# Kernel optimization log

Measured on AMD Instinct MI355X. Metric: run time of the kernel, lower is better.

Reference implementation:

```python
import jax, jax.numpy as jnp
import numpy as np

# model dims (DeepSeekV2-Lite-like, reduced expert count)
H = 2048      # hidden_dim
NH = 16       # num_heads
NOPE = 128    # qk_nope_head_dim
ROPE = 64     # qk_rope_head_dim (interleaved rotary)
VD = 128      # v_head_dim
QL = 1536     # q_lora_rank
KVL = 512     # kv_lora_rank
E = 8         # num routed experts
TOPK = 2      # num_experts_per_token
MI = 512      # moe_intermediate_dim
SH_I = 2 * MI # num_shared_experts * moe_intermediate_dim
B = 1
S = 2048
T = B * S
EPS = 1e-6
MOE_SCALE = 1.0  # gating_scaling_factor


def setup_inputs() -> dict:
    key = jax.random.key(0)
    ks = jax.random.split(key, 16)
    def w(k, shape):
        return jax.random.normal(k, shape, dtype=jnp.float32) * 0.02
    # interleaved rotary tables: one angle per (even,odd) pair
    half = ROPE // 2
    pos = jnp.arange(S, dtype=jnp.float32)
    inv_freq = 1.0 / (10000.0 ** (jnp.arange(half, dtype=jnp.float32) * 2.0 / ROPE))
    ang = pos[:, None] * inv_freq[None, :]              # [S, half]
    sin = jnp.tile(jnp.sin(ang), (B, 1))                # [T, half]
    cos = jnp.tile(jnp.cos(ang), (B, 1))
    return {
        "x": jax.random.normal(ks[0], (T, H), jnp.float32),
        "skip": jax.random.normal(ks[1], (T, H), jnp.float32),
        "rotary_sin": sin,
        "rotary_cos": cos,
        "ln1_w": jnp.ones((H,), jnp.float32),
        "ln2_w": jnp.ones((H,), jnp.float32),
        "w_qa": w(ks[2], (QL, H)),
        "qa_norm_w": jnp.ones((QL,), jnp.float32),
        "w_qb": w(ks[3], (NH * (NOPE + ROPE), QL)),
        "w_kva": w(ks[4], (KVL + ROPE, H)),
        "kva_norm_w": jnp.ones((KVL,), jnp.float32),
        "w_kb": w(ks[5], (NH * NOPE, KVL)),
        "w_vb": w(ks[6], (NH * VD, KVL)),
        "w_o": w(ks[7], (H, NH * VD)),
        "gate_w": w(ks[8], (E, H)),
        "moe_up_w": w(ks[9], (E, 2 * MI, H)),
        "moe_down_w": w(ks[10], (E, H, MI)),
        "shared_up_w": w(ks[11], (2 * SH_I, H)),
        "shared_down_w": w(ks[12], (H, SH_I)),
        "batch": B,
    }


def _rms(v, w):
    return v * jax.lax.rsqrt(jnp.mean(v * v, axis=-1, keepdims=True) + EPS) * w


def _rope_interleaved(v, sin, cos):
    # v: [T, nh, ROPE]; sin/cos: [T, ROPE//2]; rotate (even, odd) pairs
    x1, x2 = v[..., 0::2], v[..., 1::2]
    s, c = sin[:, None, :], cos[:, None, :]
    o1 = x1 * c - x2 * s
    o2 = x1 * s + x2 * c
    return jnp.stack([o1, o2], axis=-1).reshape(v.shape)


def reference(x, skip, rotary_sin, rotary_cos, ln1_w, ln2_w, w_qa, qa_norm_w,
              w_qb, w_kva, kva_norm_w, w_kb, w_vb, w_o, gate_w,
              moe_up_w, moe_down_w, shared_up_w, shared_down_w, batch):
    Tt = x.shape[0]
    Sq = Tt // batch
    # SkipRMSNorm #1
    x1 = x + skip
    n1 = _rms(x1, ln1_w)
    # ---- MLA attention (prefill path, decoding_batches=0) ----
    qa = _rms(n1 @ w_qa.T, qa_norm_w)                               # [T, QL]
    q = (qa @ w_qb.T).reshape(Tt, NH, NOPE + ROPE)
    q_nope, q_pe = q[..., :NOPE], q[..., NOPE:]
    q_pe = _rope_interleaved(q_pe, rotary_sin, rotary_cos)
    kv = n1 @ w_kva.T                                               # [T, KVL+ROPE]
    ckv = _rms(kv[:, :KVL], kva_norm_w)
    k_pe = _rope_interleaved(kv[:, KVL:][:, None, :], rotary_sin, rotary_cos)  # [T,1,ROPE]
    k_nope = (ckv @ w_kb.T).reshape(Tt, NH, NOPE)
    v = (ckv @ w_vb.T).reshape(Tt, NH, VD)
    qf = jnp.concatenate([q_nope, q_pe], -1).reshape(batch, Sq, NH, NOPE + ROPE)
    kf = jnp.concatenate([k_nope, jnp.broadcast_to(k_pe, (Tt, NH, ROPE))], -1)
    kf = kf.reshape(batch, Sq, NH, NOPE + ROPE)
    vf = v.reshape(batch, Sq, NH, VD)
    scale = 1.0 / np.sqrt(NOPE + ROPE)
    scores = jnp.einsum('bqhd,bkhd->bhqk', qf, kf) * scale
    causal = jnp.tril(jnp.ones((Sq, Sq), bool))
    scores = jnp.where(causal[None, None], scores, jnp.float32(-1e30))
    p = jax.nn.softmax(scores, axis=-1)
    o = jnp.einsum('bhqk,bkhd->bqhd', p, vf).reshape(Tt, NH * VD)
    attn = o @ w_o.T
    # SkipRMSNorm #2
    x2 = x1 + attn
    n2 = _rms(x2, ln2_w)
    # ---- MoE FFN: softmax gate, greedy top-k, normalized probs ----
    probs = jax.nn.softmax(n2 @ gate_w.T, axis=-1)                  # [T, E]
    tv, ti = jax.lax.top_k(probs, TOPK)
    tv = tv / jnp.sum(tv, axis=-1, keepdims=True) * MOE_SCALE
    routed = jnp.zeros_like(n2)
    for e in range(E):  # fixed small expert count; masked dense dispatch
        we = jnp.sum(tv * (ti == e), axis=-1)                       # [T]
        h = n2 @ moe_up_w[e].T                                      # [T, 2*MI]
        h = jax.nn.silu(h[:, :MI]) * h[:, MI:]
        routed = routed + we[:, None] * (h @ moe_down_w[e].T)
    # shared experts (dense swiglu MLP)
    hs = n2 @ shared_up_w.T
    hs = jax.nn.silu(hs[:, :SH_I]) * hs[:, SH_I:]
    ffn = routed + hs @ shared_down_w.T
    return (x2, ffn)
```

## Files before the change

### kernel.cpp

```cpp
#include <hip/hip_runtime.h>
#include <hip/hip_bf16.h>

#define H 2048
#define NH 16
#define NOPE 128
#define ROPE_D 64
#define DQK 192
#define VD 128
#define QL 1536
#define KVL 512
#define NE 8
#define MI_D 512
#define SHI 1024
#define EPS 1e-6f
#define MAXA 5120

typedef unsigned short bfu;
typedef short bf16x8 __attribute__((ext_vector_type(8)));
typedef float f32x4 __attribute__((ext_vector_type(4)));

#define MFMA16(a, b, c) __builtin_amdgcn_mfma_f32_16x16x32_bf16(a, b, c, 0, 0, 0)

#define BAR_PLAIN()   asm volatile("s_barrier" ::: "memory")
#define BAR_LGKM0()   asm volatile("s_waitcnt lgkmcnt(0)\n\ts_barrier" ::: "memory")
#define BAR_VM4()     asm volatile("s_waitcnt vmcnt(4)\n\ts_barrier" ::: "memory")
#define BAR_VM0()     asm volatile("s_waitcnt vmcnt(0)\n\ts_barrier" ::: "memory")

__device__ __forceinline__ float bf2f(bfu u) {
    union { unsigned int i; float f; } w; w.i = ((unsigned int)u) << 16; return w.f;
}
__device__ __forceinline__ bfu f2bf(float f) {
    union { float f; unsigned int i; } u; u.f = f;
    return (bfu)((u.i + 0x7fffu + ((u.i >> 16) & 1u)) >> 16);
}

__device__ __forceinline__ void async16(const bfu* g, bfu* l) {
    __builtin_amdgcn_global_load_lds((const __attribute__((address_space(1))) void*)g,
                                     (__attribute__((address_space(3))) void*)l, 16, 0, 0);
}

__device__ __forceinline__ float blk_sum(float v) {
    __shared__ float sb[4];
    for (int o = 32; o > 0; o >>= 1) v += __shfl_down(v, o, 64);
    int lane = threadIdx.x & 63, w = threadIdx.x >> 6;
    __syncthreads();
    if (lane == 0) sb[w] = v;
    __syncthreads();
    return sb[0] + sb[1] + sb[2] + sb[3];
}

struct GemmSeg {
    const bfu* A; const bfu* B; void* C; void* C2;
    const int* aidx; const int* eid;
    long bstride;
    int N, K, ldm3, mode, nx, ntiles;
};

__device__ __forceinline__ void gemm_body(const bfu* __restrict__ A, const bfu* __restrict__ B,
                                          void* __restrict__ Cv, void* __restrict__ Cv2,
                                          int N, int K, int ldm3, int mode,
                                          const int* __restrict__ aidx,
                                          const int* __restrict__ eid, long bstride,
                                          int bx, int by,
                                          bfu* sAb, bfu* sBb) {
    bfu (*sA)[128 * 32] = (bfu (*)[128 * 32])sAb;
    bfu (*sB)[128 * 32] = (bfu (*)[128 * 32])sBb;
    const int tid = threadIdx.x;
    const int lane = tid & 63, w = tid >> 6;
    const int quad = lane >> 4, li = lane & 15;
    const int m0 = by * 128, n0 = bx * 128;
    const bfu* Bp = B + (eid ? (size_t)eid[by] * bstride : 0);

    const int l4 = lane >> 2;
    const int lg = lane & 3;
    const int kc = lg ^ ((lane >> 3) & 3);
    int r0 = m0 + w * 32 + l4, r1 = r0 + 16;
    if (aidx) { r0 = aidx[r0]; r1 = aidx[r1]; }
    const bfu* gA0 = A + (size_t)r0 * K + kc * 8;
    const bfu* gA1 = A + (size_t)r1 * K + kc * 8;
    const bfu* gB0 = Bp + (size_t)(n0 + w * 32 + l4) * K + kc * 8;
    const bfu* gB1 = gB0 + (size_t)16 * K;
    const int oA0 = (w * 32) * 32, oA1 = (w * 32 + 16) * 32;

    const int wm = (w >> 1) * 64, wn = (w & 1) * 64;
    const int fg = (quad ^ ((li >> 1) & 3)) * 8;
    int oa[4], ob[4];
#pragma unroll
    for (int t4 = 0; t4 < 4; ++t4) {
        oa[t4] = (wm + t4 * 16 + li) * 32 + fg;
        ob[t4] = (wn + t4 * 16 + li) * 32 + fg;
    }
    f32x4 acc[4][4];
#pragma unroll
    for (int i = 0; i < 4; ++i)
#pragma unroll
        for (int j = 0; j < 4; ++j) acc[i][j] = (f32x4){0.f, 0.f, 0.f, 0.f};

    const int nb = K / 32;
    async16(gA0, &sA[0][oA0]); async16(gA1, &sA[0][oA1]);
    async16(gB0, &sB[0][oA0]); async16(gB1, &sB[0][oA1]);
    async16(gA0 + 32, &sA[1][oA0]); async16(gA1 + 32, &sA[1][oA1]);
    async16(gB0 + 32, &sB[1][oA0]); async16(gB1 + 32, &sB[1][oA1]);

    int cur = 0;
    for (int it = 0; it < nb; ++it) {
        if (it < nb - 1) { BAR_VM4(); } else { BAR_VM0(); }
        bf16x8 av[4], bv[4];
#pragma unroll
        for (int t4 = 0; t4 < 4; ++t4) av[t4] = *(const bf16x8*)&sA[cur][oa[t4]];
#pragma unroll
        for (int t4 = 0; t4 < 4; ++t4) bv[t4] = *(const bf16x8*)&sB[cur][ob[t4]];
        if (it + 2 < nb) {
            const int k1 = (it + 2) * 32;
            int nxt = cur + 2; if (nxt >= 3) nxt -= 3;
            async16(gA0 + k1, &sA[nxt][oA0]); async16(gA1 + k1, &sA[nxt][oA1]);
            async16(gB0 + k1, &sB[nxt][oA0]); async16(gB1 + k1, &sB[nxt][oA1]);
        }
#pragma unroll
        for (int mt = 0; mt < 4; ++mt)
#pragma unroll
            for (int nt = 0; nt < 4; ++nt)
                acc[mt][nt] = MFMA16(av[mt], bv[nt], acc[mt][nt]);
        if (++cur >= 3) cur = 0;
    }

#pragma unroll
    for (int mt = 0; mt < 4; ++mt)
#pragma unroll
        for (int nt = 0; nt < 4; ++nt) {
            int row = m0 + wm + mt * 16 + quad * 4;
            int col = n0 + wn + nt * 16 + li;
            if (mode == 0) {
                float* C = (float*)Cv;
#pragma unroll
                for (int r = 0; r < 4; ++r) C[(size_t)(row + r) * N + col] = acc[mt][nt][r];
            } else if (mode == 1) {
                bfu* C = (bfu*)Cv;
#pragma unroll
                for (int r = 0; r < 4; ++r) C[(size_t)(row + r) * N + col] = f2bf(acc[mt][nt][r]);
            } else {
                if (n0 < 2048) {
                    bfu* C = (bfu*)Cv;
#pragma unroll
                    for (int r = 0; r < 4; ++r) C[(size_t)(row + r) * 2048 + col] = f2bf(acc[mt][nt][r]);
                } else {
                    bfu* C2 = (bfu*)Cv2;
                    ushort4 u;
                    u.x = f2bf(acc[mt][nt][0]); u.y = f2bf(acc[mt][nt][1]);
                    u.z = f2bf(acc[mt][nt][2]); u.w = f2bf(acc[mt][nt][3]);
                    *(ushort4*)(C2 + (size_t)(col - 2048) * ldm3 + row) = u;
                }
            }
        }
}

__global__ __launch_bounds__(256) void gemm_multi(GemmSeg s0, GemmSeg s1) {
    __shared__ bfu sA[3][128 * 32];
    __shared__ bfu sB[3][128 * 32];
    int b = blockIdx.x;
    if (b < s0.ntiles) {
        gemm_body(s0.A, s0.B, s0.C, s0.C2, s0.N, s0.K, s0.ldm3, s0.mode,
                  s0.aidx, s0.eid, s0.bstride, b % s0.nx, b / s0.nx, &sA[0][0], &sB[0][0]);
    } else {
        int lb = b - s0.ntiles;
        gemm_body(s1.A, s1.B, s1.C, s1.C2, s1.N, s1.K, s1.ldm3, s1.mode,
                  s1.aidx, s1.eid, s1.bstride, lb % s1.nx, lb / s1.nx, &sA[0][0], &sB[0][0]);
    }
}

struct CastArgs {
    const float* s[10];
    bfu* d[10];
    unsigned start[11];
    int pad[10];
};
__global__ __launch_bounds__(256) void k_cast_all(CastArgs a) {
    unsigned g = blockIdx.x * 256 + threadIdx.x;
    if (g >= a.start[10]) return;
    int id = 0;
#pragma unroll
    for (int i = 1; i < 10; ++i) if (g >= a.start[i]) id = i;
    size_t i16 = (size_t)(g - a.start[id]) * 16;
    ushort4 u[4] = {};
    if (!a.pad[id] || (i16 >> 11) < 576) {
        const float* s = a.s[id];
#pragma unroll
        for (int j = 0; j < 4; ++j) {
            float4 x = *(const float4*)(s + i16 + j * 4);
            u[j].x = f2bf(x.x); u[j].y = f2bf(x.y); u[j].z = f2bf(x.z); u[j].w = f2bf(x.w);
        }
    }
    bfu* d = a.d[id];
#pragma unroll
    for (int j = 0; j < 4; ++j) *(ushort4*)(d + i16 + j * 4) = u[j];
}

__global__ __launch_bounds__(256) void k_add_rms(const float* __restrict__ x, const float* __restrict__ skip,
                                                 const float* __restrict__ w,
                                                 float* __restrict__ x1, bfu* __restrict__ n1b) {
    int t = blockIdx.x;
    size_t base = (size_t)t * H;
    float loc[8]; float ss = 0.f;
#pragma unroll
    for (int i = 0; i < 8; ++i) {
        int c = threadIdx.x + i * 256;
        float v = x[base + c] + skip[base + c];
        loc[i] = v; ss += v * v;
        x1[base + c] = v;
    }
    float tot = blk_sum(ss);
    float r = rsqrtf(tot / (float)H + EPS);
#pragma unroll
    for (int i = 0; i < 8; ++i) {
        int c = threadIdx.x + i * 256;
        n1b[base + c] = f2bf(loc[i] * r * w[c]);
    }
}

__global__ __launch_bounds__(256) void k_qkv_post(const bfu* __restrict__ qkv,
                                                  const float* __restrict__ qa_nw,
                                                  const float* __restrict__ kva_nw,
                                                  const float* __restrict__ sin_, const float* __restrict__ cos_,
                                                  bfu* __restrict__ qab, bfu* __restrict__ ckv,
                                                  bfu* __restrict__ kpe) {
    int t = blockIdx.x;
    const bfu* row = qkv + (size_t)t * 2176;
    float qa[6]; float ss1 = 0.f;
#pragma unroll
    for (int i = 0; i < 6; ++i) {
        float v = bf2f(row[threadIdx.x + i * 256]); qa[i] = v; ss1 += v * v;
    }
    float v0 = bf2f(row[1536 + threadIdx.x]), v1 = bf2f(row[1792 + threadIdx.x]);
    float s1 = blk_sum(ss1);
    float s2 = blk_sum(v0 * v0 + v1 * v1);
    float r1 = rsqrtf(s1 / (float)QL + EPS);
    float r2 = rsqrtf(s2 / 512.f + EPS);
#pragma unroll
    for (int i = 0; i < 6; ++i) {
        int c = threadIdx.x + i * 256;
        qab[(size_t)t * QL + c] = f2bf(qa[i] * r1 * qa_nw[c]);
    }
    ckv[(size_t)t * 512 + threadIdx.x]       = f2bf(v0 * r2 * kva_nw[threadIdx.x]);
    ckv[(size_t)t * 512 + threadIdx.x + 256] = f2bf(v1 * r2 * kva_nw[threadIdx.x + 256]);
    if (threadIdx.x < 32) {
        int p = threadIdx.x;
        float x1v = bf2f(row[2048 + 2 * p]), x2v = bf2f(row[2048 + 2 * p + 1]);
        float s = sin_[t * 32 + p], c = cos_[t * 32 + p];
        kpe[(size_t)t * 64 + 2 * p]     = f2bf(x1v * c - x2v * s);
        kpe[(size_t)t * 64 + 2 * p + 1] = f2bf(x1v * s + x2v * c);
    }
}

__global__ __launch_bounds__(256) void k_flash_mfma(const bfu* __restrict__ qb,
                                                    const bfu* __restrict__ kn,
                                                    const bfu* __restrict__ kpe,
                                                    const bfu* __restrict__ vt,
                                                    bfu* __restrict__ O,
                                                    const float* __restrict__ rsin,
                                                    const float* __restrict__ rcos, int T) {
    __shared__ bfu Ks[64 * 200];
    __shared__ bfu VtL[2][128 * 32];
    __shared__ bfu P[64 * 72];
    const int tid = threadIdx.x;
    const int lane = tid & 63, w = tid >> 6;
    const int quad = lane >> 4, li = lane & 15;
    const int q0 = ((int)gridDim.x - 1 - (int)blockIdx.x) * 64;
    const int h = blockIdx.y;
    const float scale = 0.07216878364870322f;

    bf16x8 qf[6];
    {
        int qrow = q0 + w * 16 + li;
        const bfu* qp = qb + ((size_t)qrow * NH + h) * DQK;
#pragma unroll
        for (int s6 = 0; s6 < 6; ++s6) {
            bf16x8 v = *(const bf16x8*)(qp + s6 * 32 + quad * 8);
            if (s6 >= 4) {
                int pb = (s6 - 4) * 16 + quad * 4;
#pragma unroll
                for (int j = 0; j < 4; ++j) {
                    float x1 = bf2f((bfu)v[2 * j]), x2 = bf2f((bfu)v[2 * j + 1]);
                    float s = rsin[qrow * 32 + pb + j], c = rcos[qrow * 32 + pb + j];
                    v[2 * j]     = (short)f2bf(x1 * c - x2 * s);
                    v[2 * j + 1] = (short)f2bf(x1 * s + x2 * c);
                }
            }
            qf[s6] = v;
        }
    }
    f32x4 accO[8];
#pragma unroll
    for (int i = 0; i < 8; ++i) accO[i] = (f32x4){0.f, 0.f, 0.f, 0.f};
    float lrow[4] = {0.f, 0.f, 0.f, 0.f};

    int kr[6], kg[6];
#pragma unroll
    for (int it = 0; it < 6; ++it) { int G = tid + it * 256; kr[it] = G / 24; kg[it] = G % 24; }
    int vn[4], vgl[4], vkc[4];
#pragma unroll
    for (int it = 0; it < 4; ++it) {
        int idx = tid + it * 256; vn[it] = idx >> 3; vgl[it] = idx & 7;
        vkc[it] = (vgl[it] & 4) | ((vgl[it] & 3) ^ ((vn[it] >> 1) & 3));
    }
    bf16x8 kreg[6], vreg[4];
#pragma unroll
    for (int it = 0; it < 6; ++it)
        kreg[it] = (kg[it] < 16) ? *(const bf16x8*)(kn + (size_t)kr[it] * (NH * 128) + h * 128 + kg[it] * 8)
                                 : *(const bf16x8*)(kpe + (size_t)kr[it] * 64 + (kg[it] - 16) * 8);
#pragma unroll
    for (int it = 0; it < 4; ++it)
        vreg[it] = *(const bf16x8*)(vt + (size_t)(h * 128 + vn[it]) * T + vkc[it] * 8);

    const int fgv = (quad ^ ((li >> 1) & 3)) * 8;
    const int kend = q0 + 64;
    for (int k0 = 0; k0 < kend; k0 += 64) {
        BAR_PLAIN();
#pragma unroll
        for (int it = 0; it < 6; ++it) *(bf16x8*)(Ks + kr[it] * 200 + kg[it] * 8) = kreg[it];
#pragma unroll
        for (int it = 0; it < 4; ++it)
            *(bf16x8*)(VtL[vgl[it] >> 2] + vn[it] * 32 + (vgl[it] & 3) * 8) = vreg[it];
        if (k0 + 64 < kend) {
            int k1 = k0 + 64;
#pragma unroll
            for (int it = 0; it < 6; ++it)
                kreg[it] = (kg[it] < 16) ? *(const bf16x8*)(kn + (size_t)(k1 + kr[it]) * (NH * 128) + h * 128 + kg[it] * 8)
                                         : *(const bf16x8*)(kpe + (size_t)(k1 + kr[it]) * 64 + (kg[it] - 16) * 8);
#pragma unroll
            for (int it = 0; it < 4; ++it)
                vreg[it] = *(const bf16x8*)(vt + (size_t)(h * 128 + vn[it]) * T + k1 + vkc[it] * 8);
        }
        BAR_LGKM0();
        f32x4 s[4];
#pragma unroll
        for (int ct = 0; ct < 4; ++ct) {
            f32x4 a = (f32x4){0.f, 0.f, 0.f, 0.f};
#pragma unroll
            for (int s6 = 0; s6 < 6; ++s6) {
                bf16x8 kf = *(const bf16x8*)(Ks + (ct * 16 + li) * 200 + s6 * 32 + quad * 8);
                a = MFMA16(qf[s6], kf, a);
            }
            s[ct] = a;
        }
#pragma unroll
        for (int ct = 0; ct < 4; ++ct)
#pragma unroll
            for (int r = 0; r < 4; ++r) {
                int row = q0 + w * 16 + quad * 4 + r;
                float p = (k0 + ct * 16 + li <= row) ? __expf(s[ct][r] * scale) : 0.f;
                s[ct][r] = p;
                lrow[r] += p;
            }
#pragma unroll
        for (int ct = 0; ct < 4; ++ct)
#pragma unroll
            for (int r = 0; r < 4; ++r)
                P[(w * 16 + quad * 4 + r) * 72 + ct * 16 + li] = f2bf(s[ct][r]);
        bf16x8 pf[2];
#pragma unroll
        for (int ks = 0; ks < 2; ++ks)
            pf[ks] = *(const bf16x8*)(P + (w * 16 + li) * 72 + ks * 32 + quad * 8);
#pragma unroll
        for (int v8 = 0; v8 < 8; ++v8)
#pragma unroll
            for (int ks = 0; ks < 2; ++ks) {
                bf16x8 vf = *(const bf16x8*)(VtL[ks] + (v8 * 16 + li) * 32 + fgv);
                accO[v8] = MFMA16(pf[ks], vf, accO[v8]);
            }
    }
#pragma unroll
    for (int r = 0; r < 4; ++r) {
        float l = lrow[r];
        l += __shfl_xor(l, 1); l += __shfl_xor(l, 2);
        l += __shfl_xor(l, 4); l += __shfl_xor(l, 8);
        lrow[r] = 1.0f / l;
    }
#pragma unroll
    for (int v8 = 0; v8 < 8; ++v8)
#pragma unroll
        for (int r = 0; r < 4; ++r) {
            float val = accO[v8][r] * lrow[r];
            O[(size_t)(q0 + w * 16 + quad * 4 + r) * (NH * 128) + h * 128 + v8 * 16 + li] = f2bf(val);
        }
}

__global__ __launch_bounds__(256) void k_x2_n2(const float* __restrict__ x1, const bfu* __restrict__ attn,
                                               const float* __restrict__ ln2w, float* __restrict__ outx2,
                                               bfu* __restrict__ n2b, const float* __restrict__ gw,
                                               int* __restrict__ eidx, float* __restrict__ wts,
                                               int* __restrict__ cnt) {
    int t = blockIdx.x;
    size_t base = (size_t)t * H;
    float loc[8]; float ss = 0.f;
#pragma unroll
    for (int i = 0; i < 8; ++i) {
        int c = threadIdx.x + i * 256;
        float vv = x1[base + c] + bf2f(attn[base + c]);
        loc[i] = vv; ss += vv * vv;
        outx2[base + c] = vv;
    }
    float tot = blk_sum(ss);
    float r = rsqrtf(tot / (float)H + EPS);
    float pe[NE] = {0.f, 0.f, 0.f, 0.f, 0.f, 0.f, 0.f, 0.f};
#pragma unroll
    for (int i = 0; i < 8; ++i) {
        int c = threadIdx.x + i * 256;
        float nv = loc[i] * r * ln2w[c];
        n2b[base + c] = f2bf(nv);
#pragma unroll
        for (int e = 0; e < NE; ++e) pe[e] += nv * gw[e * H + c];
    }
    __shared__ float sred[4][NE];
    int lane = threadIdx.x & 63, wv = threadIdx.x >> 6;
#pragma unroll
    for (int e = 0; e < NE; ++e) {
        float v = pe[e];
        for (int o = 32; o > 0; o >>= 1) v += __shfl_down(v, o, 64);
        if (lane == 0) sred[wv][e] = v;
    }
    __syncthreads();
    if (threadIdx.x == 0) {
        float logits[NE];
        float m = -1e30f;
        for (int e = 0; e < NE; ++e) {
            logits[e] = sred[0][e] + sred[1][e] + sred[2][e] + sred[3][e];
            m = fmaxf(m, logits[e]);
        }
        float p[NE];
        for (int e = 0; e < NE; ++e) p[e] = __expf(logits[e] - m);
        int i1 = 0;
        for (int e = 1; e < NE; ++e) if (p[e] > p[i1]) i1 = e;
        int i2 = -1;
        for (int e = 0; e < NE; ++e) if (e != i1 && (i2 < 0 || p[e] > p[i2])) i2 = e;
        float denom = p[i1] + p[i2];
        eidx[t * 2] = i1; eidx[t * 2 + 1] = i2;
        wts[t * 2] = p[i1] / denom; wts[t * 2 + 1] = p[i2] / denom;
        atomicAdd(&cnt[i1], 1); atomicAdd(&cnt[i2], 1);
    }
}

__global__ __launch_bounds__(256) void k_moe_init(int* __restrict__ cnt, int* __restrict__ slot,
                                                  int* __restrict__ eid, int* __restrict__ idx,
                                                  float* __restrict__ aw) {
    int tid = threadIdx.x;
    if (tid < NE) { cnt[tid] = 0; slot[tid] = 0; }
    if (tid < 40) eid[tid] = 0;
    for (int i = tid; i < MAXA; i += 256) { idx[i] = 0; aw[i] = 0.f; }
}

__global__ __launch_bounds__(64) void k_moe_scan(const int* __restrict__ cnt, int* __restrict__ base,
                                                 int* __restrict__ eid) {
    if (threadIdx.x == 0) {
        int off = 0;
        for (int e = 0; e < NE; ++e) {
            base[e] = off;
            int nb = (cnt[e] + 127) >> 7;
            for (int j = 0; j < nb; ++j) eid[(off >> 7) + j] = e;
            off += nb << 7;
        }
    }
}

__global__ __launch_bounds__(256) void k_moe_scatter(const int* __restrict__ eidx, const float* __restrict__ wts,
                                                     const int* __restrict__ base, int* __restrict__ slot,
                                                     int* __restrict__ idx, float* __restrict__ aw,
                                                     int* __restrict__ posmap) {
    int t = blockIdx.x * 256 + threadIdx.x;
#pragma unroll
    for (int j = 0; j < 2; ++j) {
        int e = eidx[t * 2 + j];
        int p = base[e] + atomicAdd(&slot[e], 1);
        idx[p] = t; aw[p] = wts[t * 2 + j]; posmap[t * 2 + j] = p;
    }
}

__global__ __launch_bounds__(256) void k_silu_both(const bfu* __restrict__ hsh, bfu* __restrict__ gsh,
                                                   const bfu* __restrict__ hsp, const float* __restrict__ aw,
                                                   bfu* __restrict__ gsp, int T) {
    int b = blockIdx.x;
    if (b < T) {
        const bfu* row = hsh + (size_t)b * 2048;
        bfu* grow = gsh + (size_t)b * 1024;
#pragma unroll
        for (int j = 0; j < 4; ++j) {
            int i = threadIdx.x + j * 256;
            float a = bf2f(row[i]), bb = bf2f(row[1024 + i]);
            grow[i] = f2bf(a / (1.0f + __expf(-a)) * bb);
        }
    } else {
        int row = b - T;
        float we = aw[row];
        const bfu* hr = hsp + (size_t)row * 1024;
        bfu* gr = gsp + (size_t)row * 512;
#pragma unroll
        for (int j = 0; j < 2; ++j) {
            int i = threadIdx.x + j * 256;
            float a = bf2f(hr[i]), bb = bf2f(hr[512 + i]);
            gr[i] = f2bf(we * a / (1.0f + __expf(-a)) * bb);
        }
    }
}

__global__ __launch_bounds__(256) void k_ffn_out(const float* __restrict__ routed, const bfu* __restrict__ dsp,
                                                 const int* __restrict__ posmap, float* __restrict__ out,
                                                 size_t TH) {
    int t = blockIdx.x;
    int p1 = posmap[t * 2], p2 = posmap[t * 2 + 1];
    const bfu* d1 = dsp + (size_t)p1 * H;
    const bfu* d2 = dsp + (size_t)p2 * H;
#pragma unroll
    for (int j = 0; j < 8; ++j) {
        int c = threadIdx.x + j * 256;
        out[TH + (size_t)t * H + c] = routed[(size_t)t * H + c] + bf2f(d1[c]) + bf2f(d2[c]);
    }
}

static inline GemmSeg mk_seg(const bfu* A, const bfu* B, void* C, void* C2,
                             const int* aidx, const int* eid, long bstride,
                             int N, int K, int ldm3, int mode, int nx, int ny) {
    GemmSeg s;
    s.A = A; s.B = B; s.C = C; s.C2 = C2; s.aidx = aidx; s.eid = eid; s.bstride = bstride;
    s.N = N; s.K = K; s.ldm3 = ldm3; s.mode = mode; s.nx = nx; s.ntiles = nx * ny;
    return s;
}

extern "C" void kernel_launch(void* const* d_in, const int* in_sizes, int n_in,
                              void* d_out, int out_size, void* d_ws, size_t ws_size,
                              hipStream_t stream) {
    const float* x      = (const float*)d_in[0];
    const float* skip   = (const float*)d_in[1];
    const float* rsin   = (const float*)d_in[2];
    const float* rcos   = (const float*)d_in[3];
    const float* ln1w   = (const float*)d_in[4];
    const float* ln2w   = (const float*)d_in[5];
    const float* w_qa   = (const float*)d_in[6];
    const float* qa_nw  = (const float*)d_in[7];
    const float* w_qb   = (const float*)d_in[8];
    const float* w_kva  = (const float*)d_in[9];
    const float* kva_nw = (const float*)d_in[10];
    const float* w_kb   = (const float*)d_in[11];
    const float* w_vb   = (const float*)d_in[12];
    const float* w_o    = (const float*)d_in[13];
    const float* gate_w = (const float*)d_in[14];
    const float* mup    = (const float*)d_in[15];
    const float* mdown  = (const float*)d_in[16];
    const float* shup   = (const float*)d_in[17];
    const float* shdown = (const float*)d_in[18];

    const int T = in_sizes[0] / H;

    bfu* WB = (bfu*)d_ws;
    bfu* wqkv_b  = WB + 0;
    bfu* wkbv_b  = WB + 4456448;
    bfu* wqb_b   = WB + 6553600;
    bfu* wo_b    = WB + 11272192;
    bfu* mup_b   = WB + 15466496;
    bfu* mdown_b = WB + 32243712;
    bfu* shup_b  = WB + 40632320;
    bfu* shdn_b  = WB + 44826624;
    const size_t WBYTES = 93847552;

    char* AB = (char*)d_ws + WBYTES;
    float* x1f    = (float*)(AB + 0);
    float* routed = (float*)(AB + 0);
    bfu*   n1b    = (bfu*)(AB + 16777216);
    bfu*   qkvb   = (bfu*)(AB + 25165824);
    bfu*   knb    = (bfu*)(AB + 25165824);
    bfu*   hsp    = (bfu*)(AB + 25165824);
    bfu*   qab    = (bfu*)(AB + 35651584);
    bfu*   gsp    = (bfu*)(AB + 35651584);
    bfu*   qbb    = (bfu*)(AB + 41943040);
    bfu*   attnb  = (bfu*)(AB + 41943040);
    bfu*   ckvb   = (bfu*)(AB + 54525952);
    bfu*   kpeb   = (bfu*)(AB + 56623104);
    char*  G      = AB + 56885248;
    int*   eidx   = (int*)(G);
    float* wts    = (float*)(G + 16384);
    int*   posmap = (int*)(G + 32768);
    int*   midx   = (int*)(G + 49152);
    float* maw    = (float*)(G + 69632);
    int*   mcnt   = (int*)(G + 90112);
    int*   mbase  = (int*)(G + 90112 + 64);
    int*   mslot  = (int*)(G + 90112 + 128);
    int*   meid   = (int*)(G + 90112 + 192);
    bfu*   ob     = (bfu*)(AB + 57016320);
    bfu*   gsb    = (bfu*)(AB + 57016320);
    bfu*   vtb    = (bfu*)(AB + 65404928);
    bfu*   hsb    = (bfu*)(AB + 65404928);
    bfu*   dsp    = (bfu*)(AB + 65404928);
    const size_t REQ = WBYTES + 86376448;
    if (ws_size < REQ) return;

    {
        CastArgs ca;
        const float* ss[10] = {w_qa, w_kva, w_kb, w_vb, w_qb, w_o, mup, mdown, shup, shdown};
        bfu* dd[10] = {wqkv_b, wqkv_b + 3145728, wkbv_b, wkbv_b + 1048576, wqb_b,
                       wo_b, mup_b, mdown_b, shup_b, shdn_b};
        unsigned n16[10] = {196608, 81920, 65536, 65536, 294912, 262144, 1048576, 524288, 262144, 131072};
        unsigned acc = 0;
        for (int i = 0; i < 10; ++i) { ca.s[i] = ss[i]; ca.d[i] = dd[i]; ca.start[i] = acc; acc += n16[i]; ca.pad[i] = (i == 1); }
        ca.start[10] = acc;
        k_cast_all<<<(acc + 255) / 256, 256, 0, stream>>>(ca);
    }

    k_add_rms<<<T, 256, 0, stream>>>(x, skip, ln1w, x1f, n1b);
    {
        GemmSeg s = mk_seg(n1b, wqkv_b, qkvb, nullptr, nullptr, nullptr, 0, 2176, H, 0, 1, 2176 / 128, T / 128);
        gemm_multi<<<s.ntiles, 256, 0, stream>>>(s, s);
    }
    k_qkv_post<<<T, 256, 0, stream>>>(qkvb, qa_nw, kva_nw, rsin, rcos, qab, ckvb, kpeb);
    {
        GemmSeg sq = mk_seg(qab, wqb_b, qbb, nullptr, nullptr, nullptr, 0, NH * DQK, QL, 0, 1, (NH * DQK) / 128, T / 128);
        GemmSeg sk = mk_seg(ckvb, wkbv_b, knb, vtb, nullptr, nullptr, 0, 4096, KVL, T, 4, 4096 / 128, T / 128);
        gemm_multi<<<sq.ntiles + sk.ntiles, 256, 0, stream>>>(sq, sk);
    }
    k_flash_mfma<<<dim3(T / 64, NH), 256, 0, stream>>>(qbb, knb, kpeb, vtb, ob, rsin, rcos, T);
    {
        GemmSeg s = mk_seg(ob, wo_b, attnb, nullptr, nullptr, nullptr, 0, H, NH * VD, 0, 1, H / 128, T / 128);
        gemm_multi<<<s.ntiles, 256, 0, stream>>>(s, s);
    }
    k_moe_init<<<1, 256, 0, stream>>>(mcnt, mslot, meid, midx, maw);
    k_x2_n2<<<T, 256, 0, stream>>>(x1f, attnb, ln2w, (float*)d_out, n1b, gate_w, eidx, wts, mcnt);
    k_moe_scan<<<1, 64, 0, stream>>>(mcnt, mbase, meid);
    k_moe_scatter<<<T / 256, 256, 0, stream>>>(eidx, wts, mbase, mslot, midx, maw, posmap);
    {
        GemmSeg ssh = mk_seg(n1b, shup_b, hsb, nullptr, nullptr, nullptr, 0, 2048, H, 0, 1, 2048 / 128, T / 128);
        GemmSeg smo = mk_seg(n1b, mup_b, hsp, nullptr, midx, meid, (long)1024 * H, 1024, H, 0, 1, 1024 / 128, MAXA / 128);
        gemm_multi<<<ssh.ntiles + smo.ntiles, 256, 0, stream>>>(ssh, smo);
    }
    k_silu_both<<<T + MAXA, 256, 0, stream>>>(hsb, gsb, hsp, maw, gsp, T);
    {
        GemmSeg ssd = mk_seg(gsb, shdn_b, routed, nullptr, nullptr, nullptr, 0, H, SHI, 0, 0, H / 128, T / 128);
        GemmSeg smd = mk_seg(gsp, mdown_b, dsp, nullptr, nullptr, meid, (long)H * MI_D, H, MI_D, 0, 1, H / 128, MAXA / 128);
        gemm_multi<<<ssd.ntiles + smd.ntiles, 256, 0, stream>>>(ssd, smd);
    }
    k_ffn_out<<<T, 256, 0, stream>>>(routed, dsp, posmap, (float*)d_out, (size_t)T * H);
}
```

Before: 638.0 us.

## Swizzle GEMM tiles across XCDs, stage transposed stores, coalesce cast, pad V LDS

Several independent changes land together. GEMM tile indices are remapped so consecutive tiles stay on the same XCD and walk M first, which aims to improve L2 reuse. The transposed V output in mode 4 is now staged through LDS and written as contiguous 16-byte rows instead of scattered 8-byte stores. The weight cast kernel switches to a per-thread float4 layout for coalesced accesses. The flash-attention V tile row stride is padded from 32 to 40 to reduce LDS bank conflicts. The LDS staging reuses the GEMM buffers, and the swizzle assumes tile counts map cleanly onto the grid.

Result: slower. 659.0 us (+3.3%).

```diff
diff --git a/kernel.cpp b/kernel.cpp
--- a/kernel.cpp
+++ b/kernel.cpp
@@ -37,6 +37,13 @@
 __device__ __forceinline__ void async16(const bfu* g, bfu* l) {
     __builtin_amdgcn_global_load_lds((const __attribute__((address_space(1))) void*)g,
                                      (__attribute__((address_space(3))) void*)l, 16, 0, 0);
+}
+
+__device__ __forceinline__ int xcd_swz(int b, int nt) {
+    int q = nt >> 3, r = nt & 7;
+    int x = b & 7, o = b >> 3;
+    int base = (x < r) ? x * (q + 1) : r * (q + 1) + (x - r) * q;
+    return base + o;
 }
 
 __device__ __forceinline__ float blk_sum(float v) {
@@ -124,6 +131,33 @@
         if (++cur >= 3) cur = 0;
     }
 
+    if (mode == 4 && n0 >= 2048) {
+        __syncthreads();
+        const int ST = 136;
+#pragma unroll
+        for (int mt = 0; mt < 4; ++mt)
+#pragma unroll
+            for (int nt = 0; nt < 4; ++nt)
+#pragma unroll
+                for (int r = 0; r < 4; ++r) {
+                    int lm = wm + mt * 16 + quad * 4 + r;
+                    int ln = wn + nt * 16 + li;
+                    bfu* p = (ln < 90) ? (sAb + ln * ST) : (sBb + (ln - 90) * ST);
+                    p[lm] = f2bf(acc[mt][nt][r]);
+                }
+        __syncthreads();
+        bfu* C2 = (bfu*)Cv2 + (size_t)(n0 - 2048) * ldm3 + m0;
+        int li16 = tid & 15, ng = tid >> 4;
+#pragma unroll
+        for (int nn = 0; nn < 8; ++nn) {
+            int n = ng + nn * 16;
+            const bfu* p = (n < 90) ? (sAb + n * ST) : (sBb + (n - 90) * ST);
+            bf16x8 v = *(const bf16x8*)(p + li16 * 8);
+            *(bf16x8*)(C2 + (size_t)n * ldm3 + li16 * 8) = v;
+        }
+        return;
+    }
+
 #pragma unroll
     for (int mt = 0; mt < 4; ++mt)
 #pragma unroll
@@ -139,17 +173,9 @@
 #pragma unroll
                 for (int r = 0; r < 4; ++r) C[(size_t)(row + r) * N + col] = f2bf(acc[mt][nt][r]);
             } else {
-                if (n0 < 2048) {
-                    bfu* C = (bfu*)Cv;
-#pragma unroll
-                    for (int r = 0; r < 4; ++r) C[(size_t)(row + r) * 2048 + col] = f2bf(acc[mt][nt][r]);
-                } else {
-                    bfu* C2 = (bfu*)Cv2;
-                    ushort4 u;
-                    u.x = f2bf(acc[mt][nt][0]); u.y = f2bf(acc[mt][nt][1]);
-                    u.z = f2bf(acc[mt][nt][2]); u.w = f2bf(acc[mt][nt][3]);
-                    *(ushort4*)(C2 + (size_t)(col - 2048) * ldm3 + row) = u;
-                }
+                bfu* C = (bfu*)Cv;
+#pragma unroll
+                for (int r = 0; r < 4; ++r) C[(size_t)(row + r) * 2048 + col] = f2bf(acc[mt][nt][r]);
             }
         }
 }
@@ -159,12 +185,16 @@
     __shared__ bfu sB[3][128 * 32];
     int b = blockIdx.x;
     if (b < s0.ntiles) {
+        int wg = xcd_swz(b, s0.ntiles);
+        int ny = s0.ntiles / s0.nx;
         gemm_body(s0.A, s0.B, s0.C, s0.C2, s0.N, s0.K, s0.ldm3, s0.mode,
-                  s0.aidx, s0.eid, s0.bstride, b % s0.nx, b / s0.nx, &sA[0][0], &sB[0][0]);
+                  s0.aidx, s0.eid, s0.bstride, wg / ny, wg % ny, &sA[0][0], &sB[0][0]);
     } else {
         int lb = b - s0.ntiles;
+        int wg = xcd_swz(lb, s1.ntiles);
+        int ny = s1.ntiles / s1.nx;
         gemm_body(s1.A, s1.B, s1.C, s1.C2, s1.N, s1.K, s1.ldm3, s1.mode,
-                  s1.aidx, s1.eid, s1.bstride, lb % s1.nx, lb / s1.nx, &sA[0][0], &sB[0][0]);
+                  s1.aidx, s1.eid, s1.bstride, wg / ny, wg % ny, &sA[0][0], &sB[0][0]);
     }
 }
 
@@ -175,24 +205,22 @@
     int pad[10];
 };
 __global__ __launch_bounds__(256) void k_cast_all(CastArgs a) {
-    unsigned g = blockIdx.x * 256 + threadIdx.x;
-    if (g >= a.start[10]) return;
-    int id = 0;
-#pragma unroll
-    for (int i = 1; i < 10; ++i) if (g >= a.start[i]) id = i;
-    size_t i16 = (size_t)(g - a.start[id]) * 16;
-    ushort4 u[4] = {};
-    if (!a.pad[id] || (i16 >> 11) < 576) {
-        const float* s = a.s[id];
-#pragma unroll
-        for (int j = 0; j < 4; ++j) {
-            float4 x = *(const float4*)(s + i16 + j * 4);
-            u[j].x = f2bf(x.x); u[j].y = f2bf(x.y); u[j].z = f2bf(x.z); u[j].w = f2bf(x.w);
-        }
-    }
-    bfu* d = a.d[id];
-#pragma unroll
-    for (int j = 0; j < 4; ++j) *(ushort4*)(d + i16 + j * 4) = u[j];
+    unsigned base = blockIdx.x * 1024 + threadIdx.x;
+#pragma unroll
+    for (int j = 0; j < 4; ++j) {
+        unsigned g = base + j * 256;
+        if (g >= a.start[10]) return;
+        int id = 0;
+#pragma unroll
+        for (int i = 1; i < 10; ++i) if (g >= a.start[i]) id = i;
+        size_t i4 = (size_t)(g - a.start[id]) * 4;
+        ushort4 u = {0, 0, 0, 0};
+        if (!a.pad[id] || (i4 >> 11) < 576) {
+            float4 x = *(const float4*)(a.s[id] + i4);
+            u.x = f2bf(x.x); u.y = f2bf(x.y); u.z = f2bf(x.z); u.w = f2bf(x.w);
+        }
+        *(ushort4*)(a.d[id] + i4) = u;
+    }
 }
 
 __global__ __launch_bounds__(256) void k_add_rms(const float* __restrict__ x, const float* __restrict__ skip,
@@ -259,7 +287,7 @@
                                                     const float* __restrict__ rsin,
                                                     const float* __restrict__ rcos, int T) {
     __shared__ bfu Ks[64 * 200];
-    __shared__ bfu VtL[2][128 * 32];
+    __shared__ bfu VtL[2][128 * 40];
     __shared__ bfu P[64 * 72];
     const int tid = threadIdx.x;
     const int lane = tid & 63, w = tid >> 6;
@@ -319,7 +347,7 @@
         for (int it = 0; it < 6; ++it) *(bf16x8*)(Ks + kr[it] * 200 + kg[it] * 8) = kreg[it];
 #pragma unroll
         for (int it = 0; it < 4; ++it)
-            *(bf16x8*)(VtL[vgl[it] >> 2] + vn[it] * 32 + (vgl[it] & 3) * 8) = vreg[it];
+            *(bf16x8*)(VtL[vgl[it] >> 2] + vn[it] * 40 + (vgl[it] & 3) * 8) = vreg[it];
         if (k0 + 64 < kend) {
             int k1 = k0 + 64;
 #pragma unroll
@@ -364,7 +392,7 @@
         for (int v8 = 0; v8 < 8; ++v8)
 #pragma unroll
             for (int ks = 0; ks < 2; ++ks) {
-                bf16x8 vf = *(const bf16x8*)(VtL[ks] + (v8 * 16 + li) * 32 + fgv);
+                bf16x8 vf = *(const bf16x8*)(VtL[ks] + (v8 * 16 + li) * 40 + fgv);
                 accO[v8] = MFMA16(pf[ks], vf, accO[v8]);
             }
     }
@@ -596,11 +624,11 @@
         const float* ss[10] = {w_qa, w_kva, w_kb, w_vb, w_qb, w_o, mup, mdown, shup, shdown};
         bfu* dd[10] = {wqkv_b, wqkv_b + 3145728, wkbv_b, wkbv_b + 1048576, wqb_b,
                        wo_b, mup_b, mdown_b, shup_b, shdn_b};
-        unsigned n16[10] = {196608, 81920, 65536, 65536, 294912, 262144, 1048576, 524288, 262144, 131072};
+        unsigned n4[10] = {786432, 327680, 262144, 262144, 1179648, 1048576, 4194304, 2097152, 1048576, 524288};
         unsigned acc = 0;
-        for (int i = 0; i < 10; ++i) { ca.s[i] = ss[i]; ca.d[i] = dd[i]; ca.start[i] = acc; acc += n16[i]; ca.pad[i] = (i == 1); }
+        for (int i = 0; i < 10; ++i) { ca.s[i] = ss[i]; ca.d[i] = dd[i]; ca.start[i] = acc; acc += n4[i]; ca.pad[i] = (i == 1); }
         ca.start[10] = acc;
-        k_cast_all<<<(acc + 255) / 256, 256, 0, stream>>>(ca);
+        k_cast_all<<<(acc + 1023) / 1024, 256, 0, stream>>>(ca);
     }
 
     k_add_rms<<<T, 256, 0, stream>>>(x, skip, ln1w, x1f, n1b);
```
